# Performance work log

Measured on AMD Instinct MI355X. Metric: run time of the kernel, lower is better.

## Reference

```python
import jax, jax.numpy as jnp
import numpy as np

INFLUENCE_RADIUS = 8  # VectorizedTrajectoryComputer default


def compute_trajectories(emb):
    # emb: [B, S, D] -> [B, S, D]
    B, S, D = emb.shape
    diffs = emb[:, 1:] - emb[:, :-1]                      # [B, S-1, D]
    mag = jnp.linalg.norm(diffs, axis=-1, keepdims=True)  # [B, S-1, 1]
    ntraj = diffs / jnp.maximum(mag, 1e-8)                # normalized trajectories
    mw = jnp.tanh(mag[..., 0])                            # magnitude weights [B, S-1]
    pos = jnp.arange(S)[:, None]                          # [S, 1]
    j = jnp.arange(S - 1)[None, :]                        # [1, S-1]
    ws = jnp.maximum(0, pos - INFLUENCE_RADIUS)           # window start per pos
    mask = (j >= ws) & (j < pos)                          # window_end = pos (pos <= S-1)
    wsz = jnp.maximum(pos - ws, 1)                        # window size (>=1 to avoid /0)
    recency = jnp.where(mask, (j - ws + 1) / wsz, 0.0).astype(emb.dtype)  # [S, S-1]
    cw = mw[:, None, :] * recency[None]                   # combined weights [B, S, S-1]
    nw = cw / jnp.maximum(cw.sum(-1, keepdims=True), 1e-8)
    return jnp.einsum('bpj,bjd->bpd', nw, ntraj)          # [B, S, D]


def setup_inputs() -> dict:
    key = jax.random.key(0)
    ks = jax.random.split(key, 6)
    B, S, D = 2, 2048, 1024
    H, K, hd = 16, 16, 64
    return {
        'x': jax.random.normal(ks[0], (B, S, D), dtype=jnp.float32),
        'qkv_w': jax.random.normal(ks[1], (3 * D, D), dtype=jnp.float32) * 0.02,
        'out_w': jax.random.normal(ks[2], (D, D), dtype=jnp.float32) * 0.02,
        'splat_centers': jax.random.normal(ks[3], (H, K, hd), dtype=jnp.float32) * 0.02,
        'splat_log_scales': jnp.zeros((H, K), dtype=jnp.float32),
        'splat_amplitudes': jnp.ones((H, K), dtype=jnp.float32),
    }


def reference(x, qkv_w, out_w, splat_centers, splat_log_scales, splat_amplitudes):
    B, S, D = x.shape
    H, K, hd = splat_centers.shape
    # trajectories (computed when trajectories=None in forward)
    traj = compute_trajectories(x)
    # qkv projection (no bias)
    qkv = x @ qkv_w.T                                      # [B, S, 3D]
    q, k, v = jnp.split(qkv, 3, axis=-1)
    def heads(t):
        return t.reshape(B, S, H, hd).transpose(0, 2, 1, 3)  # [B, H, S, hd]
    q, k, v = heads(q), heads(k), heads(v)
    # squared distances to splat centers: [B, H, S, K]
    cn = jnp.sum(splat_centers ** 2, axis=-1)              # [H, K]
    def dists_sq(t):
        tn = jnp.sum(t ** 2, axis=-1, keepdims=True)       # [B, H, S, 1]
        cross = jnp.einsum('bhsd,hkd->bhsk', t, splat_centers)
        return tn - 2.0 * cross + cn[None, :, None, :]
    scales_sq = jnp.exp(splat_log_scales)[None, :, None, :] ** 2  # [1, H, 1, K]
    amp = jax.nn.sigmoid(splat_amplitudes)[None, :, None, :]
    q_weights = jnp.exp(-0.5 * dists_sq(q) / scales_sq) * amp     # [B, H, S, K]
    k_weights = jnp.exp(-0.5 * dists_sq(k) / scales_sq) * amp
    attn = jnp.einsum('bhis,bhjs->bhij', q_weights, k_weights)    # [B, H, S, S]
    attn = jax.nn.softmax(attn, axis=-1)
    out = jnp.einsum('bhij,bhjd->bhid', attn, v)                  # [B, H, S, hd]
    out = out.transpose(0, 2, 1, 3).reshape(B, S, D) @ out_w.T    # [B, S, D]
    return out, traj
```

## Files before the change

### kernel.cpp

```cpp
#include <hip/hip_runtime.h>
#include <math.h>

#define SEQ 2048
#define DIM 1024
#define NB  2
#define NH  16

typedef __attribute__((ext_vector_type(8))) short short8;
typedef __attribute__((ext_vector_type(4))) float floatx4;
typedef __attribute__((ext_vector_type(16))) float floatx16;

__device__ __forceinline__ ushort f2bf(float f) {
    unsigned u = __float_as_uint(f);
    return (ushort)((u + 0x7FFFu + ((u >> 16) & 1u)) >> 16);
}
__device__ __forceinline__ float bf2f(ushort h) {
    return __uint_as_float(((unsigned)h) << 16);
}
__device__ __forceinline__ void gload16(const void* g, char* lds_base) {
    __builtin_amdgcn_global_load_lds(
        (const __attribute__((address_space(1))) void*)g,
        (__attribute__((address_space(3))) void*)lds_base, 16, 0, 0);
}
__device__ __forceinline__ unsigned cvtpk(float a, float b) {
    unsigned r;
    asm("v_cvt_pk_bf16_f32 %0, %1, %2" : "=v"(r) : "v"(a), "v"(b));
    return r;
}
__device__ __forceinline__ void plswap(unsigned &a, unsigned &b) {
    asm("v_permlane32_swap_b32 %0, %1" : "+v"(a), "+v"(b));
}

__global__ __launch_bounds__(256) void cvt_hi_kernel(
    const float* __restrict__ src, ushort* __restrict__ dst, int n)
{
    int i = (blockIdx.x * 256 + threadIdx.x) * 4;
    if (i >= n) return;
    float4 v = *(const float4*)(src + i);
    ushort4 o;
    o.x = f2bf(v.x); o.y = f2bf(v.y); o.z = f2bf(v.z); o.w = f2bf(v.w);
    *(ushort4*)(dst + i) = o;
}

__global__ __launch_bounds__(256) void cvt_split_kernel(
    const float* __restrict__ src, ushort* __restrict__ hi, ushort* __restrict__ lo, int n)
{
    int i = (blockIdx.x * 256 + threadIdx.x) * 4;
    if (i >= n) return;
    float4 v = *(const float4*)(src + i);
    ushort4 h, l;
    h.x = f2bf(v.x); l.x = f2bf(v.x - bf2f(h.x));
    h.y = f2bf(v.y); l.y = f2bf(v.y - bf2f(h.y));
    h.z = f2bf(v.z); l.z = f2bf(v.z - bf2f(h.z));
    h.w = f2bf(v.w); l.w = f2bf(v.w - bf2f(h.w));
    *(ushort4*)(hi + i) = h;
    *(ushort4*)(lo + i) = l;
}

__global__ __launch_bounds__(256) void traj_stats_kernel(
    const float* __restrict__ x, float* __restrict__ sbuf, float* __restrict__ invbuf)
{
    const int wave = threadIdx.x >> 6;
    const int lane = threadIdx.x & 63;
    const int row  = blockIdx.x * 4 + wave;
    const int NR = NB * (SEQ - 1);
    if (row >= NR) return;
    const int b = row / (SEQ - 1);
    const int j = row - b * (SEQ - 1);
    const float* x0 = x + ((size_t)(b * SEQ + j)) * DIM;
    const float* x1 = x0 + DIM;
    float sum = 0.f;
    #pragma unroll
    for (int q = 0; q < 4; ++q) {
        int idx = q * 256 + lane * 4;
        float4 a = *(const float4*)(x0 + idx);
        float4 c = *(const float4*)(x1 + idx);
        float dx = c.x-a.x, dy = c.y-a.y, dz = c.z-a.z, dw = c.w-a.w;
        sum += dx*dx + dy*dy + dz*dz + dw*dw;
    }
    #pragma unroll
    for (int off = 32; off > 0; off >>= 1) sum += __shfl_down(sum, off);
    if (lane == 0) {
        float mag = sqrtf(sum);
        sbuf[row]   = tanhf(mag);
        invbuf[row] = 1.0f / fmaxf(mag, 1e-8f);
    }
}

__global__ __launch_bounds__(256) void traj_kernel(
    const float* __restrict__ x, const float* __restrict__ sbuf,
    const float* __restrict__ invbuf, float* __restrict__ traj_out)
{
    const int bp = blockIdx.x;
    const int b  = bp >> 11;
    const int p  = bp & (SEQ - 1);
    int ws = p - 8; if (ws < 0) ws = 0;
    const int wlen = p - ws;
    const float wsz = (float)((p - ws) > 1 ? (p - ws) : 1);
    const int base = b * (SEQ - 1) + ws;

    float Z = 0.f;
    for (int t = 0; t < wlen; ++t)
        Z += sbuf[base + t] * ((float)(t + 1) / wsz);
    const float scale = 1.0f / fmaxf(Z, 1e-8f);

    const int d0 = threadIdx.x * 4;
    const float* xb = x + ((size_t)(b * SEQ + ws)) * DIM + d0;
    float4 prev = *(const float4*)xb;
    float4 acc = make_float4(0.f,0.f,0.f,0.f);
    for (int t = 0; t < wlen; ++t) {
        xb += DIM;
        float4 cur = *(const float4*)xb;
        float cc = sbuf[base + t] * ((float)(t + 1) / wsz) * invbuf[base + t] * scale;
        acc.x += cc * (cur.x - prev.x);
        acc.y += cc * (cur.y - prev.y);
        acc.z += cc * (cur.z - prev.z);
        acc.w += cc * (cur.w - prev.w);
        prev = cur;
    }
    *(float4*)(traj_out + (size_t)bp * DIM + d0) = acc;
}

template<int SPLIT, int EPI>
__global__ __launch_bounds__(256) void mfma_gemm(
    const ushort* __restrict__ Ah, const ushort* __restrict__ Al,
    const ushort* __restrict__ Bh, const ushort* __restrict__ Bl,
    float* __restrict__ cout, int ldc,
    ushort* __restrict__ qwb, ushort* __restrict__ kwb)
{
    constexpr int SMEM = SPLIT ? 32768 : 16384;
    __shared__ char smem[SMEM];
    const int tid = threadIdx.x;
    const int l = tid & 63;
    const int w = tid >> 6;
    const int wm = w >> 1, wn = w & 1;
    const int n0 = blockIdx.x * 128;
    const int m0 = blockIdx.y * 128;

    char* a_h = smem;
    char* b_h = smem + 8192;
    char* a_l = smem + 16384;
    char* b_l = smem + 24576;

    const int srow = 32 * w + (l >> 2);
    const int scol = (l & 3) * 8;
    const ushort* Ahg = Ah + (size_t)(m0 + srow) * 1024 + scol;
    const ushort* Bhg = Bh + (size_t)(n0 + srow) * 1024 + scol;
    const ushort* Alg = SPLIT ? Al + (size_t)(m0 + srow) * 1024 + scol : nullptr;
    const ushort* Blg = SPLIT ? Bl + (size_t)(n0 + srow) * 1024 + scol : nullptr;

    floatx4 acc[4][4] = {};
    const int fr = l & 15;
    const int fq = (l >> 4) * 16;

    for (int kb = 0; kb < 1024; kb += 32) {
        if (kb) __syncthreads();
        gload16(Ahg + kb,             a_h + w*2048);
        gload16(Ahg + kb + 16*1024,   a_h + w*2048 + 1024);
        gload16(Bhg + kb,             b_h + w*2048);
        gload16(Bhg + kb + 16*1024,   b_h + w*2048 + 1024);
        if (SPLIT) {
            gload16(Alg + kb,           a_l + w*2048);
            gload16(Alg + kb + 16*1024, a_l + w*2048 + 1024);
            gload16(Blg + kb,           b_l + w*2048);
            gload16(Blg + kb + 16*1024, b_l + w*2048 + 1024);
        }
        __syncthreads();
        short8 fah[4], fbh[4], fal[4], fbl[4];
        #pragma unroll
        for (int t = 0; t < 4; ++t) {
            fah[t] = *(const short8*)(a_h + ((wm*64 + t*16 + fr) << 6) + fq);
            fbh[t] = *(const short8*)(b_h + ((wn*64 + t*16 + fr) << 6) + fq);
            if (SPLIT) {
                fal[t] = *(const short8*)(a_l + ((wm*64 + t*16 + fr) << 6) + fq);
                fbl[t] = *(const short8*)(b_l + ((wn*64 + t*16 + fr) << 6) + fq);
            }
        }
        #pragma unroll
        for (int it = 0; it < 4; ++it)
            #pragma unroll
            for (int jt = 0; jt < 4; ++jt) {
                acc[it][jt] = __builtin_amdgcn_mfma_f32_16x16x32_bf16(
                    fah[it], fbh[jt], acc[it][jt], 0, 0, 0);
                if (SPLIT) {
                    acc[it][jt] = __builtin_amdgcn_mfma_f32_16x16x32_bf16(
                        fah[it], fbl[jt], acc[it][jt], 0, 0, 0);
                    acc[it][jt] = __builtin_amdgcn_mfma_f32_16x16x32_bf16(
                        fal[it], fbh[jt], acc[it][jt], 0, 0, 0);
                }
            }
    }

    const int row0 = (l >> 4) * 4;
    const int col  = l & 15;

    if (EPI == 0) {
        #pragma unroll
        for (int it = 0; it < 4; ++it)
            #pragma unroll
            for (int jt = 0; jt < 4; ++jt)
                #pragma unroll
                for (int r = 0; r < 4; ++r) {
                    int gm = m0 + wm*64 + it*16 + row0 + r;
                    int gn = n0 + wn*64 + jt*16 + col;
                    cout[(size_t)gm * ldc + gn] = acc[it][jt][r];
                }
    } else if (EPI == 2) {
        #pragma unroll
        for (int it = 0; it < 4; ++it)
            #pragma unroll
            for (int jt = 0; jt < 4; ++jt)
                #pragma unroll
                for (int r = 0; r < 4; ++r) {
                    int md = m0 + wm*64 + it*16 + row0 + r;
                    int t  = n0 + wn*64 + jt*16 + col;
                    int bb = t >> 11, ss = t & (SEQ - 1);
                    qwb[((size_t)bb << 21) + (size_t)md * SEQ + ss] = f2bf(acc[it][jt][r]);
                }
    } else {
        ushort* obuf = (n0 < 1024) ? qwb : kwb;
        const int nb = n0 & 1023;
        #pragma unroll
        for (int it = 0; it < 4; ++it)
            #pragma unroll
            for (int jt = 0; jt < 4; ++jt)
                #pragma unroll
                for (int r = 0; r < 4; ++r) {
                    int gm = m0 + wm*64 + it*16 + row0 + r;
                    int gn = nb + wn*64 + jt*16 + col;
                    int hh = gn >> 6, d = gn & 63;
                    int bb = gm >> 11, ss = gm & (SEQ - 1);
                    obuf[(((size_t)(bb*NH + hh))*SEQ + ss)*64 + d] = f2bf(acc[it][jt][r]);
                }
    }
}

__global__ __launch_bounds__(256) void splat_kernel(
    const ushort* __restrict__ qk, ushort* __restrict__ wout,
    const float* __restrict__ centers, const float* __restrict__ lscales,
    const float* __restrict__ amps)
{
    __shared__ float Cs[16*64];
    __shared__ float Pr[48];
    const int tid = threadIdx.x;
    const int bh  = blockIdx.x >> 3;
    const int h   = bh & 15;
    const int s   = (blockIdx.x & 7) * 256 + tid;
    {
        float4 c4 = *(const float4*)(centers + (size_t)h*1024 + tid*4);
        *(float4*)(Cs + tid*4) = c4;
    }
    if (tid < 16) {
        float s2 = __expf(2.f * lscales[h*16 + tid]);
        Pr[tid]      = -0.5f / s2;
        Pr[16 + tid] = 1.f / (1.f + __expf(-amps[h*16 + tid]));
        const float* cp = centers + ((size_t)h*16 + tid)*64;
        float cn = 0.f;
        for (int i = 0; i < 64; ++i) cn += cp[i]*cp[i];
        Pr[32 + tid] = cn;
    }
    __syncthreads();

    float q[64];
    const ushort* qp = qk + ((size_t)bh*SEQ + s)*64;
    #pragma unroll
    for (int i = 0; i < 8; ++i) {
        short8 v = *(const short8*)(qp + i*8);
        #pragma unroll
        for (int j = 0; j < 8; ++j) q[i*8+j] = bf2f((ushort)v[j]);
    }
    float tn = 0.f;
    #pragma unroll
    for (int i = 0; i < 64; ++i) tn = fmaf(q[i], q[i], tn);

    ushort o16[16];
    #pragma unroll 4
    for (int sp = 0; sp < 16; ++sp) {
        const float* cp = Cs + sp*64;
        float cr = 0.f;
        #pragma unroll
        for (int i = 0; i < 64; ++i) cr = fmaf(q[i], cp[i], cr);
        float dq = tn - 2.f*cr + Pr[32 + sp];
        o16[sp] = f2bf(__expf(dq * Pr[sp]) * Pr[16 + sp]);
    }
    ushort* op = wout + ((size_t)bh*SEQ + s)*16;
    *(short8*)(op)     = *(short8*)(o16);
    *(short8*)(op + 8) = *(short8*)(o16 + 8);
}

__global__ __launch_bounds__(256, 4) void attn_kernel(
    const ushort* __restrict__ qw, const ushort* __restrict__ kw,
    const ushort* __restrict__ vbt, ushort* __restrict__ hoh, ushort* __restrict__ hol)
{
    __shared__ __align__(16) char smem[16384 + 512];
    const int tid = threadIdx.x;
    const int l   = tid & 63;
    const int w   = tid >> 6;
    const int qh  = w >> 1;
    const int kh  = w & 1;
    const int l31 = l & 31;
    const int hi  = l >> 5;
    const int bh = blockIdx.y;
    const int b = bh >> 4;
    const int h = bh & 15;
    const int s0 = blockIdx.x * 64;

    short8 qf = *(const short8*)(qw + ((size_t)bh*SEQ + s0 + qh*32 + l31)*16 + hi*8);

    const ushort* kfp = kw + ((size_t)bh*SEQ + kh*32 + l31)*16 + hi*8;
    const ushort* vtb = vbt + ((size_t)(b*1024 + h*64))*SEQ;

    const int dA = w*16 + (l >> 3);
    const int dB = dA + 8;
    const ushort* vsA = vtb + (size_t)dA*SEQ + ((l & 7) ^ (dA & 7))*8;
    const ushort* vsB = vtb + (size_t)dB*SEQ + ((l & 7) ^ (dB & 7))*8;

    floatx16 acc0 = {}, acc1 = {};
    floatx16 zero16 = {};
    float zpart = 0.f;

    gload16(vsA, smem + w*2048);
    gload16(vsB, smem + w*2048 + 1024);
    short8 kf = *(const short8*)kfp;

    for (int jt = 0; jt < 32; ++jt) {
        __syncthreads();
        char* bufn = smem + ((jt + 1) & 1)*8192;
        if (jt < 31) {
            gload16(vsA + (jt + 1)*64, bufn + w*2048);
            gload16(vsB + (jt + 1)*64, bufn + w*2048 + 1024);
        }
        floatx16 sc = __builtin_amdgcn_mfma_f32_32x32x16_bf16(kf, qf, zero16, 0, 0, 0);
        if (jt < 31) kf = *(const short8*)(kfp + (jt + 1)*1024);

        float e[16];
        #pragma unroll
        for (int r = 0; r < 16; ++r) e[r] = __expf(sc[r]);
        float zs = 0.f;
        #pragma unroll
        for (int r = 0; r < 16; ++r) zs += e[r];
        zpart += zs;

        unsigned p0 = cvtpk(e[0],  e[1]),  p1 = cvtpk(e[2],  e[3]);
        unsigned p2 = cvtpk(e[4],  e[5]),  p3 = cvtpk(e[6],  e[7]);
        unsigned p4 = cvtpk(e[8],  e[9]),  p5 = cvtpk(e[10], e[11]);
        unsigned p6 = cvtpk(e[12], e[13]), p7 = cvtpk(e[14], e[15]);
        plswap(p0, p2); plswap(p1, p3);
        plswap(p4, p6); plswap(p5, p7);
        union { unsigned u[4]; short8 s; } ua, ub;
        ua.u[0] = p0; ua.u[1] = p1; ua.u[2] = p2; ua.u[3] = p3;
        ub.u[0] = p4; ub.u[1] = p5; ub.u[2] = p6; ub.u[3] = p7;

        const ushort* buf = (const ushort*)(smem + (jt & 1)*8192);
        #pragma unroll
        for (int dt = 0; dt < 2; ++dt) {
            int row = dt*32 + l31;
            const ushort* vr = buf + row*64;
            int bk0 = (kh*4 + hi)     ^ (row & 7);
            int bk1 = (kh*4 + 2 + hi) ^ (row & 7);
            short8 vb0 = *(const short8*)(vr + bk0*8);
            short8 vb1 = *(const short8*)(vr + bk1*8);
            if (dt == 0) {
                acc0 = __builtin_amdgcn_mfma_f32_32x32x16_bf16(ua.s, vb0, acc0, 0, 0, 0);
                acc0 = __builtin_amdgcn_mfma_f32_32x32x16_bf16(ub.s, vb1, acc0, 0, 0, 0);
            } else {
                acc1 = __builtin_amdgcn_mfma_f32_32x32x16_bf16(ua.s, vb0, acc1, 0, 0, 0);
                acc1 = __builtin_amdgcn_mfma_f32_32x32x16_bf16(ub.s, vb1, acc1, 0, 0, 0);
            }
        }
    }

    __syncthreads();

    float* cb = (float*)smem;
    float* zb = (float*)(smem + 16384);

    unsigned za = __float_as_uint(zpart), zc = za;
    plswap(za, zc);
    float zq = __uint_as_float(za) + __uint_as_float(zc);
    if (l31 == l) zb[kh*64 + qh*32 + l31] = zq;

    if (kh) {
        #pragma unroll
        for (int r = 0; r < 16; ++r) {
            int q = (r & 3) + 8*(r >> 2) + 4*hi;
            cb[(qh*32 + q)*64 + l31]      = acc0[r];
            cb[(qh*32 + q)*64 + 32 + l31] = acc1[r];
        }
    }
    __syncthreads();
    if (!kh) {
        #pragma unroll
        for (int r = 0; r < 16; ++r) {
            int q = (r & 3) + 8*(r >> 2) + 4*hi;
            float zt = zb[qh*32 + q] + zb[64 + qh*32 + q];
            float inv = 1.0f / zt;
            int s = s0 + qh*32 + q;
            size_t base = ((size_t)(b*SEQ + s))*1024 + h*64;
            float v0 = (acc0[r] + cb[(qh*32 + q)*64 + l31])      * inv;
            float v1 = (acc1[r] + cb[(qh*32 + q)*64 + 32 + l31]) * inv;
            ushort h0 = f2bf(v0);
            ushort h1 = f2bf(v1);
            hoh[base + l31]      = h0;
            hol[base + l31]      = f2bf(v0 - bf2f(h0));
            hoh[base + 32 + l31] = h1;
            hol[base + 32 + l31] = f2bf(v1 - bf2f(h1));
        }
    }
}

extern "C" void kernel_launch(void* const* d_in, const int* in_sizes, int n_in,
                              void* d_out, int out_size, void* d_ws, size_t ws_size,
                              hipStream_t stream)
{
    const float* x       = (const float*)d_in[0];
    const float* qkv_w   = (const float*)d_in[1];
    const float* out_w   = (const float*)d_in[2];
    const float* centers = (const float*)d_in[3];
    const float* lscales = (const float*)d_in[4];
    const float* amps    = (const float*)d_in[5];
    float* out  = (float*)d_out;
    float* traj = out + (size_t)NB*SEQ*DIM;

    char* wsb = (char*)d_ws;
    ushort* xh   = (ushort*)(wsb);
    ushort* xl   = (ushort*)(wsb + (8u<<20));
    ushort* wh   = (ushort*)(wsb + (16u<<20));
    ushort* wlv  = (ushort*)(wsb + (22u<<20));
    ushort* vbt  = (ushort*)(wsb + (24u<<20));
    float*  sbuf = (float*)(wsb + (40u<<20));
    float*  invb = sbuf + 4096;
    ushort* qbuf = xl;
    ushort* kbuf = (ushort*)(wsb + (32u<<20));
    ushort* qwbh = wlv;
    ushort* kwbh = wh + 2048*1024;
    ushort* owh  = wh;
    ushort* owl  = wh + 1048576;
    ushort* hoh  = xh;
    ushort* hol  = xl;

    cvt_split_kernel<<<4096, 256, 0, stream>>>(x, xh, xl, 4194304);
    cvt_hi_kernel<<<3072, 256, 0, stream>>>(qkv_w, wh, 3145728);
    cvt_split_kernel<<<1024, 256, 0, stream>>>(qkv_w + 2097152, wh + 2097152, wlv, 1048576);
    traj_stats_kernel<<<1024, 256, 0, stream>>>(x, sbuf, invb);
    traj_kernel<<<NB*SEQ, 256, 0, stream>>>(x, sbuf, invb, traj);
    mfma_gemm<1,2><<<dim3(32, 8), 256, 0, stream>>>(
        wh + 2048*1024, wlv, xh, xl, nullptr, 0, vbt, nullptr);
    mfma_gemm<0,3><<<dim3(16, 32), 256, 0, stream>>>(
        xh, nullptr, wh, nullptr, nullptr, 0, qbuf, kbuf);
    splat_kernel<<<256, 256, 0, stream>>>(qbuf, qwbh, centers, lscales, amps);
    splat_kernel<<<256, 256, 0, stream>>>(kbuf, kwbh, centers, lscales, amps);
    cvt_split_kernel<<<1024, 256, 0, stream>>>(out_w, owh, owl, 1048576);
    attn_kernel<<<dim3(32, 32), 256, 0, stream>>>(qwbh, kwbh, vbt, hoh, hol);
    mfma_gemm<1,0><<<dim3(8, 32), 256, 0, stream>>>(
        hoh, hol, owh, owl, out, 1024, nullptr, nullptr);
}
```

Baseline: 290.4 us.

## Merge conversion and splat launches, halve GEMM N-tile for more blocks

Folds the three front-end fp32-to-bf16 conversion kernels into a single launch, and merges the separate Q and K splat launches into one grid. Adds a BN template parameter to the MFMA GEMM and uses 64-wide N tiles for the V projection and output projection, doubling their block counts (256 to 512) to fill more compute units on a 256-CU-class GPU. The smaller tiles lower per-block reuse of the A operand and add global traffic, in exchange for better occupancy and fewer launches.

```diff
diff --git a/kernel.cpp b/kernel.cpp
--- a/kernel.cpp
+++ b/kernel.cpp
@@ -29,17 +29,6 @@
 }
 __device__ __forceinline__ void plswap(unsigned &a, unsigned &b) {
     asm("v_permlane32_swap_b32 %0, %1" : "+v"(a), "+v"(b));
-}
-
-__global__ __launch_bounds__(256) void cvt_hi_kernel(
-    const float* __restrict__ src, ushort* __restrict__ dst, int n)
-{
-    int i = (blockIdx.x * 256 + threadIdx.x) * 4;
-    if (i >= n) return;
-    float4 v = *(const float4*)(src + i);
-    ushort4 o;
-    o.x = f2bf(v.x); o.y = f2bf(v.y); o.z = f2bf(v.z); o.w = f2bf(v.w);
-    *(ushort4*)(dst + i) = o;
 }
 
 __global__ __launch_bounds__(256) void cvt_split_kernel(
@@ -55,6 +44,41 @@
     h.w = f2bf(v.w); l.w = f2bf(v.w - bf2f(h.w));
     *(ushort4*)(hi + i) = h;
     *(ushort4*)(lo + i) = l;
+}
+
+__global__ __launch_bounds__(256) void cvt_front_kernel(
+    const float* __restrict__ x, const float* __restrict__ qkv_w,
+    ushort* __restrict__ xh, ushort* __restrict__ xl,
+    ushort* __restrict__ wh, ushort* __restrict__ wlv)
+{
+    const int blk = blockIdx.x;
+    if (blk < 4096) {
+        int i = blk * 1024 + threadIdx.x * 4;
+        float4 v = *(const float4*)(x + i);
+        ushort4 h, l;
+        h.x = f2bf(v.x); l.x = f2bf(v.x - bf2f(h.x));
+        h.y = f2bf(v.y); l.y = f2bf(v.y - bf2f(h.y));
+        h.z = f2bf(v.z); l.z = f2bf(v.z - bf2f(h.z));
+        h.w = f2bf(v.w); l.w = f2bf(v.w - bf2f(h.w));
+        *(ushort4*)(xh + i) = h;
+        *(ushort4*)(xl + i) = l;
+    } else if (blk < 6144) {
+        int i = (blk - 4096) * 1024 + threadIdx.x * 4;
+        float4 v = *(const float4*)(qkv_w + i);
+        ushort4 o;
+        o.x = f2bf(v.x); o.y = f2bf(v.y); o.z = f2bf(v.z); o.w = f2bf(v.w);
+        *(ushort4*)(wh + i) = o;
+    } else {
+        int i = (blk - 6144) * 1024 + threadIdx.x * 4;
+        float4 v = *(const float4*)(qkv_w + 2097152 + i);
+        ushort4 h, l;
+        h.x = f2bf(v.x); l.x = f2bf(v.x - bf2f(h.x));
+        h.y = f2bf(v.y); l.y = f2bf(v.y - bf2f(h.y));
+        h.z = f2bf(v.z); l.z = f2bf(v.z - bf2f(h.z));
+        h.w = f2bf(v.w); l.w = f2bf(v.w - bf2f(h.w));
+        *(ushort4*)(wh + 2097152 + i) = h;
+        *(ushort4*)(wlv + i) = l;
+    }
 }
 
 __global__ __launch_bounds__(256) void traj_stats_kernel(
@@ -121,35 +145,39 @@
     *(float4*)(traj_out + (size_t)bp * DIM + d0) = acc;
 }
 
-template<int SPLIT, int EPI>
+template<int SPLIT, int EPI, int BN>
 __global__ __launch_bounds__(256) void mfma_gemm(
     const ushort* __restrict__ Ah, const ushort* __restrict__ Al,
     const ushort* __restrict__ Bh, const ushort* __restrict__ Bl,
     float* __restrict__ cout, int ldc,
     ushort* __restrict__ qwb, ushort* __restrict__ kwb)
 {
-    constexpr int SMEM = SPLIT ? 32768 : 16384;
-    __shared__ char smem[SMEM];
+    constexpr int JT   = BN / 32;
+    constexpr int BSZ  = BN * 64;
+    constexpr int HALF = 8192 + BSZ;
+    constexpr int SMEM = (SPLIT ? 2 : 1) * HALF;
+    __shared__ __align__(16) char smem[SMEM];
     const int tid = threadIdx.x;
     const int l = tid & 63;
     const int w = tid >> 6;
     const int wm = w >> 1, wn = w & 1;
-    const int n0 = blockIdx.x * 128;
+    const int n0 = blockIdx.x * BN;
     const int m0 = blockIdx.y * 128;
 
     char* a_h = smem;
     char* b_h = smem + 8192;
-    char* a_l = smem + 16384;
-    char* b_l = smem + 24576;
-
-    const int srow = 32 * w + (l >> 2);
-    const int scol = (l & 3) * 8;
-    const ushort* Ahg = Ah + (size_t)(m0 + srow) * 1024 + scol;
-    const ushort* Bhg = Bh + (size_t)(n0 + srow) * 1024 + scol;
-    const ushort* Alg = SPLIT ? Al + (size_t)(m0 + srow) * 1024 + scol : nullptr;
-    const ushort* Blg = SPLIT ? Bl + (size_t)(n0 + srow) * 1024 + scol : nullptr;
-
-    floatx4 acc[4][4] = {};
+    char* a_l = smem + HALF;
+    char* b_l = smem + HALF + 8192;
+
+    const int srowA = 32 * w + (l >> 2);
+    const int srowB = (BN == 128 ? 32 * w : 16 * w) + (l >> 2);
+    const int scol  = (l & 3) * 8;
+    const ushort* Ahg = Ah + (size_t)(m0 + srowA) * 1024 + scol;
+    const ushort* Bhg = Bh + (size_t)(n0 + srowB) * 1024 + scol;
+    const ushort* Alg = SPLIT ? Al + (size_t)(m0 + srowA) * 1024 + scol : nullptr;
+    const ushort* Blg = SPLIT ? Bl + (size_t)(n0 + srowB) * 1024 + scol : nullptr;
+
+    floatx4 acc[4][JT] = {};
     const int fr = l & 15;
     const int fq = (l >> 4) * 16;
 
@@ -157,29 +185,40 @@
         if (kb) __syncthreads();
         gload16(Ahg + kb,             a_h + w*2048);
         gload16(Ahg + kb + 16*1024,   a_h + w*2048 + 1024);
-        gload16(Bhg + kb,             b_h + w*2048);
-        gload16(Bhg + kb + 16*1024,   b_h + w*2048 + 1024);
+        if (BN == 128) {
+            gload16(Bhg + kb,             b_h + w*2048);
+            gload16(Bhg + kb + 16*1024,   b_h + w*2048 + 1024);
+        } else {
+            gload16(Bhg + kb,             b_h + w*1024);
+        }
         if (SPLIT) {
             gload16(Alg + kb,           a_l + w*2048);
             gload16(Alg + kb + 16*1024, a_l + w*2048 + 1024);
-            gload16(Blg + kb,           b_l + w*2048);
-            gload16(Blg + kb + 16*1024, b_l + w*2048 + 1024);
+            if (BN == 128) {
+                gload16(Blg + kb,           b_l + w*2048);
+                gload16(Blg + kb + 16*1024, b_l + w*2048 + 1024);
+            } else {
+                gload16(Blg + kb,           b_l + w*1024);
+            }
         }
         __syncthreads();
-        short8 fah[4], fbh[4], fal[4], fbl[4];
+        short8 fah[4], fbh[JT], fal[4], fbl[JT];
         #pragma unroll
         for (int t = 0; t < 4; ++t) {
             fah[t] = *(const short8*)(a_h + ((wm*64 + t*16 + fr) << 6) + fq);
-            fbh[t] = *(const short8*)(b_h + ((wn*64 + t*16 + fr) << 6) + fq);
-            if (SPLIT) {
+            if (SPLIT)
                 fal[t] = *(const short8*)(a_l + ((wm*64 + t*16 + fr) << 6) + fq);
-                fbl[t] = *(const short8*)(b_l + ((wn*64 + t*16 + fr) << 6) + fq);
-            }
+        }
+        #pragma unroll
+        for (int t = 0; t < JT; ++t) {
+            fbh[t] = *(const short8*)(b_h + ((wn*(BN/2) + t*16 + fr) << 6) + fq);
+            if (SPLIT)
+                fbl[t] = *(const short8*)(b_l + ((wn*(BN/2) + t*16 + fr) << 6) + fq);
         }
         #pragma unroll
         for (int it = 0; it < 4; ++it)
             #pragma unroll
-            for (int jt = 0; jt < 4; ++jt) {
+            for (int jt = 0; jt < JT; ++jt) {
                 acc[it][jt] = __builtin_amdgcn_mfma_f32_16x16x32_bf16(
                     fah[it], fbh[jt], acc[it][jt], 0, 0, 0);
                 if (SPLIT) {
@@ -198,22 +237,22 @@
         #pragma unroll
         for (int it = 0; it < 4; ++it)
             #pragma unroll
-            for (int jt = 0; jt < 4; ++jt)
+            for (int jt = 0; jt < JT; ++jt)
                 #pragma unroll
                 for (int r = 0; r < 4; ++r) {
                     int gm = m0 + wm*64 + it*16 + row0 + r;
-                    int gn = n0 + wn*64 + jt*16 + col;
+                    int gn = n0 + wn*(BN/2) + jt*16 + col;
                     cout[(size_t)gm * ldc + gn] = acc[it][jt][r];
                 }
     } else if (EPI == 2) {
         #pragma unroll
         for (int it = 0; it < 4; ++it)
             #pragma unroll
-            for (int jt = 0; jt < 4; ++jt)
+            for (int jt = 0; jt < JT; ++jt)
                 #pragma unroll
                 for (int r = 0; r < 4; ++r) {
                     int md = m0 + wm*64 + it*16 + row0 + r;
-                    int t  = n0 + wn*64 + jt*16 + col;
+                    int t  = n0 + wn*(BN/2) + jt*16 + col;
                     int bb = t >> 11, ss = t & (SEQ - 1);
                     qwb[((size_t)bb << 21) + (size_t)md * SEQ + ss] = f2bf(acc[it][jt][r]);
                 }
@@ -223,11 +262,11 @@
         #pragma unroll
         for (int it = 0; it < 4; ++it)
             #pragma unroll
-            for (int jt = 0; jt < 4; ++jt)
+            for (int jt = 0; jt < JT; ++jt)
                 #pragma unroll
                 for (int r = 0; r < 4; ++r) {
                     int gm = m0 + wm*64 + it*16 + row0 + r;
-                    int gn = nb + wn*64 + jt*16 + col;
+                    int gn = nb + wn*(BN/2) + jt*16 + col;
                     int hh = gn >> 6, d = gn & 63;
                     int bb = gm >> 11, ss = gm & (SEQ - 1);
                     obuf[(((size_t)(bb*NH + hh))*SEQ + ss)*64 + d] = f2bf(acc[it][jt][r]);
@@ -236,16 +275,21 @@
 }
 
 __global__ __launch_bounds__(256) void splat_kernel(
-    const ushort* __restrict__ qk, ushort* __restrict__ wout,
+    const ushort* __restrict__ qin, const ushort* __restrict__ kin,
+    ushort* __restrict__ wq, ushort* __restrict__ wk,
     const float* __restrict__ centers, const float* __restrict__ lscales,
     const float* __restrict__ amps)
 {
     __shared__ float Cs[16*64];
     __shared__ float Pr[48];
     const int tid = threadIdx.x;
-    const int bh  = blockIdx.x >> 3;
+    const int isK = blockIdx.x >> 8;
+    const int bx  = blockIdx.x & 255;
+    const ushort* qk = isK ? kin : qin;
+    ushort* wout = isK ? wk : wq;
+    const int bh  = bx >> 3;
     const int h   = bh & 15;
-    const int s   = (blockIdx.x & 7) * 256 + tid;
+    const int s   = (bx & 7) * 256 + tid;
     {
         float4 c4 = *(const float4*)(centers + (size_t)h*1024 + tid*4);
         *(float4*)(Cs + tid*4) = c4;
@@ -439,19 +483,16 @@
     ushort* hoh  = xh;
     ushort* hol  = xl;
 
-    cvt_split_kernel<<<4096, 256, 0, stream>>>(x, xh, xl, 4194304);
-    cvt_hi_kernel<<<3072, 256, 0, stream>>>(qkv_w, wh, 3145728);
-    cvt_split_kernel<<<1024, 256, 0, stream>>>(qkv_w + 2097152, wh + 2097152, wlv, 1048576);
+    cvt_front_kernel<<<7168, 256, 0, stream>>>(x, qkv_w, xh, xl, wh, wlv);
     traj_stats_kernel<<<1024, 256, 0, stream>>>(x, sbuf, invb);
     traj_kernel<<<NB*SEQ, 256, 0, stream>>>(x, sbuf, invb, traj);
-    mfma_gemm<1,2><<<dim3(32, 8), 256, 0, stream>>>(
+    mfma_gemm<1,2,64><<<dim3(64, 8), 256, 0, stream>>>(
         wh + 2048*1024, wlv, xh, xl, nullptr, 0, vbt, nullptr);
-    mfma_gemm<0,3><<<dim3(16, 32), 256, 0, stream>>>(
+    mfma_gemm<0,3,128><<<dim3(16, 32), 256, 0, stream>>>(
         xh, nullptr, wh, nullptr, nullptr, 0, qbuf, kbuf);
-    splat_kernel<<<256, 256, 0, stream>>>(qbuf, qwbh, centers, lscales, amps);
-    splat_kernel<<<256, 256, 0, stream>>>(kbuf, kwbh, centers, lscales, amps);
+    splat_kernel<<<512, 256, 0, stream>>>(qbuf, kbuf, qwbh, kwbh, centers, lscales, amps);
     cvt_split_kernel<<<1024, 256, 0, stream>>>(out_w, owh, owl, 1048576);
     attn_kernel<<<dim3(32, 32), 256, 0, stream>>>(qwbh, kwbh, vbt, hoh, hol);
-    mfma_gemm<1,0><<<dim3(8, 32), 256, 0, stream>>>(
+    mfma_gemm<1,0,64><<<dim3(16, 32), 256, 0, stream>>>(
         hoh, hol, owh, owl, out, 1024, nullptr, nullptr);
 }
```

Result: faster. 270.5 us (-6.9%).
